# Performance work log

Measured on AMD Instinct MI355X. Metric: run time of the kernel, lower is better.

The kernel has to match this reference:

```python
import jax, jax.numpy as jnp
import numpy as np

NIBBLE_ZERO = 8  # int4 zero-point (symmetric around 8 for unsigned nibble storage)


def _dequant(w_packed, w_scales):
    # w_packed: [out, in//2] int32 holding uint8 bytes, two 4-bit values each.
    low = w_packed & 0xF            # first nibble -> even input positions
    high = (w_packed >> 4) & 0xF    # second nibble -> odd input positions
    out_f = w_packed.shape[0]
    # interleave nibbles along the input dim: [out, in//2, 2] -> [out, in]
    q = jnp.stack([low, high], axis=-1).reshape(out_f, -1)
    return (q.astype(w_scales.dtype) - NIBBLE_ZERO) * w_scales[:, None]  # [out, in]


def setup_inputs() -> dict:
    key = jax.random.key(0)
    k1, k2, k3, k4 = jax.random.split(key, 4)
    N, IN, OUT = 4096, 4096, 4096
    x = jax.random.normal(k1, (N, IN), dtype=jnp.float32)
    w_packed = jax.random.randint(k2, (OUT, IN // 2), 0, 256, dtype=jnp.int32)
    w_scales = jax.random.uniform(k3, (OUT,), dtype=jnp.float32, minval=0.01, maxval=0.05)
    bias = jax.random.normal(k4, (OUT,), dtype=jnp.float32)
    return {"x": x, "w_packed": w_packed, "w_scales": w_scales, "bias": bias}


def reference(x, w_packed, w_scales, bias):
    W = _dequant(w_packed, w_scales)          # [out, in]
    return jnp.einsum('ni,oi->no', x, W) + bias  # [N, out]
```

## Files before the change

kernel.cpp:

```cpp
#include <hip/hip_runtime.h>
#include <hip/hip_bf16.h>


typedef __attribute__((ext_vector_type(8))) __bf16 bf16x8;
typedef __attribute__((ext_vector_type(4))) float f32x4;

#define GLOBAL_AS __attribute__((address_space(1)))
#define LDS_AS __attribute__((address_space(3)))

#define BM 256
#define BN 256
#define BK 64

__device__ inline unsigned short f32_to_bf16(float f) {
    unsigned int u = __float_as_uint(f);
    unsigned int r = (u + 0x7FFFu + ((u >> 16) & 1u)) >> 16;
    return (unsigned short)r;
}

__global__ void prep(const float* __restrict__ x, unsigned short* __restrict__ xb,
                     const int* __restrict__ wp, unsigned short* __restrict__ wb,
                     int n8x, int n4w) {
    const int stride = gridDim.x * blockDim.x;
    const int total = n8x + n4w;
    for (int i = blockIdx.x * blockDim.x + threadIdx.x; i < total; i += stride) {
        if (i < n8x) {
            float4 a = ((const float4*)x)[2 * i];
            float4 b = ((const float4*)x)[2 * i + 1];
            union { unsigned short h[8]; uint4 u; } o;
            o.h[0] = f32_to_bf16(a.x); o.h[1] = f32_to_bf16(a.y);
            o.h[2] = f32_to_bf16(a.z); o.h[3] = f32_to_bf16(a.w);
            o.h[4] = f32_to_bf16(b.x); o.h[5] = f32_to_bf16(b.y);
            o.h[6] = f32_to_bf16(b.z); o.h[7] = f32_to_bf16(b.w);
            ((uint4*)xb)[i] = o.u;
        } else {
            const int li = i - n8x;
            const int l  = li & 63;
            const int W  = li >> 6;
            const int jb = W >> 7;
            const int gb = W & 127;
            const int am = l & 15, g4 = l >> 4;
            const int o_ = jb * 16 + am;
            const int g  = gb * 4 + g4;
            int4 v = ((const int4*)wp)[(size_t)o_ * 512 + g];
            int vals[4] = {v.x, v.y, v.z, v.w};
            union { unsigned short h[8]; uint4 u; } u8;
#pragma unroll
            for (int t2 = 0; t2 < 4; ++t2) {
                u8.h[2 * t2]     = f32_to_bf16((float)((vals[t2] & 0xF) - 8));
                u8.h[2 * t2 + 1] = f32_to_bf16((float)(((vals[t2] >> 4) & 0xF) - 8));
            }
            const int t_ = g >> 3, kk_ = (g >> 2) & 1, aq_ = g & 3;
            ((uint4*)wb)[(jb << 13) | (t_ << 7) | (kk_ << 6) | (aq_ << 4) | am] = u8.u;
        }
    }
}

template<int K, int N>
__global__ __launch_bounds__(512, 2) void gemm_bt(
    const unsigned short* __restrict__ A,
    const unsigned short* __restrict__ Bf,
    const float* __restrict__ scales,
    const float* __restrict__ bias,
    float* __restrict__ C,
    int GY)
{
    constexpr int NT = K / BK;
    __shared__ __align__(16) unsigned short lds[32768];

    const int tid  = threadIdx.x;
    const int wave = tid >> 6;
    const int lane = tid & 63;
    const int wm = wave >> 2;
    const int wn = wave & 3;

    const int bid = blockIdx.x;
    const int chunk = gridDim.x >> 3;
    const int sw = (bid & 7) * chunk + (bid >> 3);
    const int bx = sw / GY;
    const int by = sw - bx * GY;
    const int m0 = by * BM;
    const int n0 = bx * BN;

    const int am = lane & 15;
    const int aq = lane >> 4;
    const int cb = ((aq ^ (am & 7)) << 4);

    int aoff[8];
#pragma unroll
    for (int i = 0; i < 8; ++i) {
        int r = (2 * i + wm) * 16 + am;
        aoff[i] = ((i < 4) ? 0 : 16384) + (r & 127) * 128 + cb;
    }

    int bpan[4];
#pragma unroll
    for (int j = 0; j < 4; ++j)
        bpan[j] = ((n0 >> 4) + 4 * j + wn) << 16;
    const int lane8 = lane * 8;

    const int sch = tid & 7;
    const int r0 = tid >> 3;
    const int r1 = (512 + tid) >> 3;
    const size_t g0 = (size_t)r0 * K + (size_t)((sch ^ (r0 & 7)) * 8);
    const size_t g1 = (size_t)r1 * K + (size_t)((sch ^ (r1 & 7)) * 8);
    const int d0 = tid * 8;
    const int d1 = (512 + tid) * 8;

    const unsigned short* Abase = A + (size_t)m0 * K;

    f32x4 acc[8][4];
#pragma unroll
    for (int i = 0; i < 8; ++i)
#pragma unroll
        for (int j = 0; j < 4; ++j)
            acc[i][j] = (f32x4){0.f, 0.f, 0.f, 0.f};

    const char* ldsB = (const char*)lds;
    bf16x8 af8[8];
    bf16x8 bX[4], bY[4];

#define STAGE(half, kcol, uoff)                                                   \
    do {                                                                          \
        const unsigned short* _g = Abase + (size_t)((half) * 128) * K + (kcol);   \
        __builtin_amdgcn_global_load_lds((const GLOBAL_AS void*)(_g + g0),        \
            (LDS_AS void*)(lds + (uoff) + d0), 16, 0, 0);                         \
        __builtin_amdgcn_global_load_lds((const GLOBAL_AS void*)(_g + g1),        \
            (LDS_AS void*)(lds + (uoff) + d1), 16, 0, 0);                         \
    } while (0)

#define LDA_KK(kkv, OBb)                                                          \
    _Pragma("unroll") for (int i2 = 0; i2 < 8; ++i2) {                            \
        af8[i2] = *(const bf16x8*)(ldsB + (OBb) + (aoff[i2] ^ ((kkv) * 64)));     \
    }

#define LDBG(dst, TT2, kkv)                                                       \
    _Pragma("unroll") for (int j2 = 0; j2 < 4; ++j2) {                            \
        dst[j2] = *(const bf16x8*)(Bf + (size_t)bpan[j2] + (TT2) * 1024           \
                                   + (kkv) * 512 + lane8);                        \
    }

#define MFMA_PH(bset)                                                             \
    _Pragma("unroll") for (int i2 = 0; i2 < 8; ++i2)                              \
    _Pragma("unroll") for (int j2 = 0; j2 < 4; ++j2)                              \
        acc[i2][j2] = __builtin_amdgcn_mfma_f32_16x16x32_bf16(                    \
            af8[i2], bset[j2], acc[i2][j2], 0, 0, 0);

#define TILE(TT, OBb, OUSo)                                                       \
    {                                                                             \
        const int tn = (((TT) + 1 < NT) ? (TT) + 1 : NT - 1);                     \
        asm volatile("s_waitcnt vmcnt(0)" ::: "memory");                          \
        __builtin_amdgcn_s_barrier();                                             \
        LDBG(bY, (TT), 1);                             \
        STAGE(0, tn * BK, (OUSo));                       \
        STAGE(1, tn * BK, (OUSo) + 8192);                                         \
        LDA_KK(0, OBb);                                                           \
        __builtin_amdgcn_s_setprio(1); MFMA_PH(bX); __builtin_amdgcn_s_setprio(0);\
        LDBG(bX, tn, 0);                            \
        LDA_KK(1, OBb);                                                           \
        __builtin_amdgcn_s_setprio(1); MFMA_PH(bY); __builtin_amdgcn_s_setprio(0);\
    }

    STAGE(0, 0, 0);
    STAGE(1, 0, 8192);
    LDBG(bX, 0, 0);

    for (int t = 0; t < NT; t += 2) {
        TILE(t, 0, 16384);
        TILE(t + 1, 32768, 0);
    }
    asm volatile("s_waitcnt vmcnt(0)" ::: "memory");

    const int cq = lane >> 4;
    const int cc = lane & 15;
#pragma unroll
    for (int j = 0; j < 4; ++j) {
        const int col = n0 + (4 * j + wn) * 16 + cc;
        const float s = scales[col];
        const float b = bias[col];
#pragma unroll
        for (int i = 0; i < 8; ++i) {
            const int rowb = m0 + (2 * i + wm) * 16 + cq * 4;
#pragma unroll
            for (int r = 0; r < 4; ++r) {
                C[(size_t)(rowb + r) * N + col] = acc[i][j][r] * s + b;
            }
        }
    }
#undef STAGE
#undef LDA_KK
#undef LDBG
#undef MFMA_PH
#undef TILE
}

__global__ void naive_kernel(const float* __restrict__ x, const int* __restrict__ wp,
                             const float* __restrict__ sc, const float* __restrict__ bs,
                             float* __restrict__ out, int NR, int OUTF, int INF) {
    int idx = blockIdx.x * 256 + threadIdx.x;
    if (idx >= NR * OUTF) return;
    int n = idx / OUTF, o = idx - n * OUTF;
    const float* xr = x + (size_t)n * INF;
    const int* wr = wp + (size_t)o * (INF / 2);
    float acc = 0.f;
    for (int c = 0; c < INF / 2; ++c) {
        int v = wr[c];
        acc += xr[2 * c] * (float)((v & 0xF) - 8) + xr[2 * c + 1] * (float)(((v >> 4) & 0xF) - 8);
    }
    out[idx] = acc * sc[o] + bs[o];
}

extern "C" void kernel_launch(void* const* d_in, const int* in_sizes, int n_in,
                              void* d_out, int out_size, void* d_ws, size_t ws_size,
                              hipStream_t stream) {
    const float* x      = (const float*)d_in[0];
    const int*   wp     = (const int*)d_in[1];
    const float* scales = (const float*)d_in[2];
    const float* bias   = (const float*)d_in[3];
    float* out = (float*)d_out;

    const int OUTF = in_sizes[2];
    const int INF  = (2 * in_sizes[1]) / OUTF;
    const int NR   = in_sizes[0] / INF;

    unsigned short* xb = (unsigned short*)d_ws;
    unsigned short* wb = xb + (size_t)NR * INF;
    const size_t need = ((size_t)NR * INF + (size_t)OUTF * INF) * sizeof(unsigned short);

    const int GX = OUTF / BN;
    const int GY = NR / BM;

    if (ws_size >= need && INF == 4096 && OUTF == 4096 && NR == 4096
        && ((GX * GY) % 8) == 0
        && (in_sizes[0] % 8) == 0 && (in_sizes[1] % 4) == 0) {
        prep<<<2048, 256, 0, stream>>>(x, xb, wp, wb, in_sizes[0] / 8, in_sizes[1] / 4);
        gemm_bt<4096, 4096><<<GX * GY, 512, 0, stream>>>(xb, wb, scales, bias, out, GY);
    } else {
        int total = NR * OUTF;
        naive_kernel<<<(total + 255) / 256, 256, 0, stream>>>(x, wp, scales, bias, out, NR, OUTF, INF);
    }
}
```

Baseline: 272.8 us.

## Switch GEMM to 32x32x16 bf16 MFMA with matching weight layout

Replaces the 16x16x32 MFMA tiling with 32x32x16 MFMA instructions. Each wave now holds 4x2 accumulators of 16 floats instead of 8x4 of 4, with new LDS A-offsets, a re-laid-out pre-swizzled weight buffer and a new epilogue row mapping. The aim is fewer MFMA issues and fewer operand loads per FLOP. It also relaxes the per-tile wait from vmcnt(0) to vmcnt(4) so the B-fragment global loads can stay in flight across the barrier, which risks a correctness hazard if the count does not match the outstanding loads.

```diff
diff --git a/kernel.cpp b/kernel.cpp
--- a/kernel.cpp
+++ b/kernel.cpp
@@ -3,7 +3,7 @@
 
 
 typedef __attribute__((ext_vector_type(8))) __bf16 bf16x8;
-typedef __attribute__((ext_vector_type(4))) float f32x4;
+typedef __attribute__((ext_vector_type(16))) float f32x16;
 
 #define GLOBAL_AS __attribute__((address_space(1)))
 #define LDS_AS __attribute__((address_space(3)))
@@ -50,8 +50,11 @@
                 u8.h[2 * t2]     = f32_to_bf16((float)((vals[t2] & 0xF) - 8));
                 u8.h[2 * t2 + 1] = f32_to_bf16((float)(((vals[t2] >> 4) & 0xF) - 8));
             }
-            const int t_ = g >> 3, kk_ = (g >> 2) & 1, aq_ = g & 3;
-            ((uint4*)wb)[(jb << 13) | (t_ << 7) | (kk_ << 6) | (aq_ << 4) | am] = u8.u;
+            const int p_ = o_ >> 5;
+            const int t_ = g >> 3;
+            const int s_ = (g >> 1) & 3;
+            const int h_ = g & 1;
+            ((uint4*)wb)[(p_ << 14) | (((t_ << 2) | s_) << 6) | (h_ << 5) | (o_ & 31)] = u8.u;
         }
     }
 }
@@ -82,21 +85,25 @@
     const int m0 = by * BM;
     const int n0 = bx * BN;
 
-    const int am = lane & 15;
-    const int aq = lane >> 4;
-    const int cb = ((aq ^ (am & 7)) << 4);
-
-    int aoff[8];
-#pragma unroll
-    for (int i = 0; i < 8; ++i) {
-        int r = (2 * i + wm) * 16 + am;
-        aoff[i] = ((i < 4) ? 0 : 16384) + (r & 127) * 128 + cb;
-    }
-
-    int bpan[4];
-#pragma unroll
-    for (int j = 0; j < 4; ++j)
-        bpan[j] = ((n0 >> 4) + 4 * j + wn) << 16;
+    const int l31 = lane & 31;
+    const int kh  = lane >> 5;
+    int aoff32[4][4];
+#pragma unroll
+    for (int mi = 0; mi < 4; ++mi) {
+        const int b  = 2 * mi + wm;
+        const int hr = (b & 3) * 32 + l31;
+        const int hbase = (b >> 2) * 16384;
+#pragma unroll
+        for (int s = 0; s < 4; ++s) {
+            const int c0 = s * 2 + kh;
+            aoff32[mi][s] = hbase + hr * 128 + (((c0 ^ (hr & 7))) << 4);
+        }
+    }
+
+    int bpan[2];
+#pragma unroll
+    for (int nj = 0; nj < 2; ++nj)
+        bpan[nj] = ((n0 >> 5) + wn * 2 + nj) << 17;
     const int lane8 = lane * 8;
 
     const int sch = tid & 7;
@@ -109,12 +116,14 @@
 
     const unsigned short* Abase = A + (size_t)m0 * K;
 
-    f32x4 acc[8][4];
-#pragma unroll
-    for (int i = 0; i < 8; ++i)
-#pragma unroll
-        for (int j = 0; j < 4; ++j)
-            acc[i][j] = (f32x4){0.f, 0.f, 0.f, 0.f};
+    f32x16 acc[4][2];
+#pragma unroll
+    for (int mi = 0; mi < 4; ++mi)
+#pragma unroll
+        for (int nj = 0; nj < 2; ++nj)
+#pragma unroll
+            for (int r = 0; r < 16; ++r)
+                acc[mi][nj][r] = 0.f;
 
     const char* ldsB = (const char*)lds;
     bf16x8 af8[8];
@@ -129,36 +138,38 @@
             (LDS_AS void*)(lds + (uoff) + d1), 16, 0, 0);                         \
     } while (0)
 
-#define LDA_KK(kkv, OBb)                                                          \
-    _Pragma("unroll") for (int i2 = 0; i2 < 8; ++i2) {                            \
-        af8[i2] = *(const bf16x8*)(ldsB + (OBb) + (aoff[i2] ^ ((kkv) * 64)));     \
-    }
-
-#define LDBG(dst, TT2, kkv)                                                       \
-    _Pragma("unroll") for (int j2 = 0; j2 < 4; ++j2) {                            \
-        dst[j2] = *(const bf16x8*)(Bf + (size_t)bpan[j2] + (TT2) * 1024           \
-                                   + (kkv) * 512 + lane8);                        \
-    }
-
-#define MFMA_PH(bset)                                                             \
-    _Pragma("unroll") for (int i2 = 0; i2 < 8; ++i2)                              \
-    _Pragma("unroll") for (int j2 = 0; j2 < 4; ++j2)                              \
-        acc[i2][j2] = __builtin_amdgcn_mfma_f32_16x16x32_bf16(                    \
-            af8[i2], bset[j2], acc[i2][j2], 0, 0, 0);
+#define LDA32(H, OBb)                                                             \
+    _Pragma("unroll") for (int mi = 0; mi < 4; ++mi)                              \
+    _Pragma("unroll") for (int ss = 0; ss < 2; ++ss)                              \
+        af8[mi * 2 + ss] =                                                        \
+            *(const bf16x8*)(ldsB + (OBb) + aoff32[mi][(H) * 2 + ss]);
+
+#define LDBG(dst, TT2, H)                                                         \
+    _Pragma("unroll") for (int nj = 0; nj < 2; ++nj)                              \
+    _Pragma("unroll") for (int ss = 0; ss < 2; ++ss)                              \
+        dst[nj * 2 + ss] = *(const bf16x8*)(Bf + bpan[nj]                         \
+            + ((((TT2) << 2) | ((H) << 1) | ss) << 9) + lane8);
+
+#define MFMA_H(bset)                                                              \
+    _Pragma("unroll") for (int ss = 0; ss < 2; ++ss)                              \
+    _Pragma("unroll") for (int mi = 0; mi < 4; ++mi)                              \
+    _Pragma("unroll") for (int nj = 0; nj < 2; ++nj)                              \
+        acc[mi][nj] = __builtin_amdgcn_mfma_f32_32x32x16_bf16(                    \
+            af8[mi * 2 + ss], bset[nj * 2 + ss], acc[mi][nj], 0, 0, 0);
 
 #define TILE(TT, OBb, OUSo)                                                       \
     {                                                                             \
         const int tn = (((TT) + 1 < NT) ? (TT) + 1 : NT - 1);                     \
-        asm volatile("s_waitcnt vmcnt(0)" ::: "memory");                          \
+        asm volatile("s_waitcnt vmcnt(4)" ::: "memory");                          \
         __builtin_amdgcn_s_barrier();                                             \
-        LDBG(bY, (TT), 1);                             \
+        LDBG(bY, (TT), 1);                        \
         STAGE(0, tn * BK, (OUSo));                       \
         STAGE(1, tn * BK, (OUSo) + 8192);                                         \
-        LDA_KK(0, OBb);                                                           \
-        __builtin_amdgcn_s_setprio(1); MFMA_PH(bX); __builtin_amdgcn_s_setprio(0);\
+        LDA32(0, OBb);                                    \
+        __builtin_amdgcn_s_setprio(1); MFMA_H(bX); __builtin_amdgcn_s_setprio(0); \
         LDBG(bX, tn, 0);                            \
-        LDA_KK(1, OBb);                                                           \
-        __builtin_amdgcn_s_setprio(1); MFMA_PH(bY); __builtin_amdgcn_s_setprio(0);\
+        LDA32(1, OBb);                                    \
+        __builtin_amdgcn_s_setprio(1); MFMA_H(bY); __builtin_amdgcn_s_setprio(0); \
     }
 
     STAGE(0, 0, 0);
@@ -171,26 +182,25 @@
     }
     asm volatile("s_waitcnt vmcnt(0)" ::: "memory");
 
-    const int cq = lane >> 4;
-    const int cc = lane & 15;
-#pragma unroll
-    for (int j = 0; j < 4; ++j) {
-        const int col = n0 + (4 * j + wn) * 16 + cc;
+#pragma unroll
+    for (int nj = 0; nj < 2; ++nj) {
+        const int col = n0 + wn * 64 + nj * 32 + l31;
         const float s = scales[col];
         const float b = bias[col];
 #pragma unroll
-        for (int i = 0; i < 8; ++i) {
-            const int rowb = m0 + (2 * i + wm) * 16 + cq * 4;
-#pragma unroll
-            for (int r = 0; r < 4; ++r) {
-                C[(size_t)(rowb + r) * N + col] = acc[i][j][r] * s + b;
+        for (int mi = 0; mi < 4; ++mi) {
+            const int rowb = m0 + (2 * mi + wm) * 32 + 4 * kh;
+#pragma unroll
+            for (int r = 0; r < 16; ++r) {
+                const int row = rowb + (r & 3) + 8 * (r >> 2);
+                C[(size_t)row * N + col] = acc[mi][nj][r] * s + b;
             }
         }
     }
 #undef STAGE
-#undef LDA_KK
+#undef LDA32
 #undef LDBG
-#undef MFMA_PH
+#undef MFMA_H
 #undef TILE
 }
 
```

Measured after the change: 278.4 us. +2.0%, slower.
